# Kernel optimization log

Measured on AMD Instinct MI355X. Metric: run time of the kernel, lower is better.

The kernel has to match this reference:

```python
import jax, jax.numpy as jnp
import numpy as np

B, N, S, D1, D2 = 4, 16384, 4096, 128, 256
C_IN = D1 + D2  # 384
MLP = [256, 256]
EPS_BN = 1e-5


def setup_inputs() -> dict:
    key = jax.random.key(0)
    ks = jax.random.split(key, 16)
    inp = {
        "points_xyz1": jax.random.normal(ks[0], (B, N, 3), dtype=jnp.float32),
        "points_xyz2": jax.random.normal(ks[1], (B, S, 3), dtype=jnp.float32),
        "points_fea1": jax.random.normal(ks[2], (B, D1, N), dtype=jnp.float32),
        "points_fea2": jax.random.normal(ks[3], (B, D2, S), dtype=jnp.float32),
    }
    c_in = C_IN
    for i, c_out in enumerate(MLP):
        scale = 1.0 / np.sqrt(c_in)
        inp[f"W{i}"] = jax.random.uniform(ks[4 + 3 * i], (c_out, c_in), jnp.float32, -scale, scale)
        inp[f"b{i}"] = jax.random.uniform(ks[5 + 3 * i], (c_out,), jnp.float32, -scale, scale)
        inp[f"gamma{i}"] = jnp.ones((c_out,), jnp.float32)
        inp[f"beta{i}"] = jnp.zeros((c_out,), jnp.float32)
        c_in = c_out
    return inp


def _coordinate_distance(x1, x2):
    # squared euclidean distance matrix: (B,N,S)
    n1 = jnp.sum(x1 * x1, axis=-1, keepdims=True)          # (B,N,1)
    n2 = jnp.sum(x2 * x2, axis=-1, keepdims=True)          # (B,S,1)
    return n1 + jnp.swapaxes(n2, 1, 2) - 2.0 * jnp.einsum("bnc,bsc->bns", x1, x2)


def _conv_bn_relu(x, W, b, gamma, beta):
    # 1x1 conv: (B,Cin,N) -> (B,Cout,N), then BatchNorm1d (training stats) + ReLU
    y = jnp.einsum("oc,bcn->bon", W, x) + b[None, :, None]
    mean = jnp.mean(y, axis=(0, 2), keepdims=True)
    var = jnp.var(y, axis=(0, 2), keepdims=True)
    y = (y - mean) * jax.lax.rsqrt(var + EPS_BN)
    y = y * gamma[None, :, None] + beta[None, :, None]
    return jax.nn.relu(y)


def reference(points_xyz1, points_xyz2, points_fea1, points_fea2,
              W0, b0, gamma0, beta0, W1, b1, gamma1, beta1):
    dists = _coordinate_distance(points_xyz1[..., :3], points_xyz2[..., :3])  # (B,N,S)
    neg_d, idx = jax.lax.top_k(-dists, 3)                                     # 3 smallest
    d3 = -neg_d                                                               # (B,N,3)
    dist_recip = 1.0 / jnp.maximum(d3, 1e-8)
    weight = dist_recip / jnp.sum(dist_recip, axis=2, keepdims=True)          # (B,N,3)
    fea2t = jnp.swapaxes(points_fea2, 1, 2)                                   # (B,S,D2)
    gathered = fea2t[jnp.arange(B)[:, None, None], idx]                       # (B,N,3,D2)
    interp = jnp.sum(gathered * weight[..., None], axis=2)                    # (B,N,D2)
    new_fea = jnp.concatenate((points_fea1, jnp.swapaxes(interp, 1, 2)), axis=1)  # (B,D1+D2,N)
    new_fea = _conv_bn_relu(new_fea, W0, b0, gamma0, beta0)
    new_fea = _conv_bn_relu(new_fea, W1, b1, gamma1, beta1)
    return new_fea
```

## Files before the change

### kernel.cpp

```cpp
#include <hip/hip_runtime.h>
#include <math.h>

namespace {

constexpr int kB = 4;
constexpr int kN = 16384;
constexpr int kS = 4096;
constexpr int kD1 = 128;
constexpr int kD2 = 256;
constexpr int kCO = 256;
constexpr int kNCOL = kB * kN;
constexpr int kKX = kD1 + kD2;

constexpr size_t kOffAb0 = 262144;
constexpr size_t kOffAb1 = 264192;
constexpr size_t kOffY0  = 266240;
constexpr size_t kOffX1  = 33820672;

typedef __bf16 bf16x8 __attribute__((ext_vector_type(8)));
typedef float f32x4 __attribute__((ext_vector_type(4)));

__device__ __forceinline__ float bf2f(unsigned short u) {
  unsigned int x = ((unsigned int)u) << 16;
  float f;
  __builtin_memcpy(&f, &x, 4);
  return f;
}
__device__ __forceinline__ unsigned short f2bf(float f) {
  unsigned int x;
  __builtin_memcpy(&x, &f, 4);
  x += 0x7fffu + ((x >> 16) & 1u);
  return (unsigned short)(x >> 16);
}

__device__ __forceinline__ void cp16_async(const void* g, void* l) {
#if __has_builtin(__builtin_amdgcn_global_load_lds)
  __builtin_amdgcn_global_load_lds(
      (const __attribute__((address_space(1))) unsigned int*)g,
      (__attribute__((address_space(3))) unsigned int*)l, 16, 0, 0);
#else
  *(uint4*)l = *(const uint4*)g;
#endif
}

__global__ __launch_bounds__(256) void pts4_kernel(const float* __restrict__ xyz2,
                                                   float4* __restrict__ pts4) {
#pragma clang fp contract(off)
  int i = blockIdx.x * 256 + threadIdx.x;
  float x = xyz2[i * 3 + 0];
  float y = xyz2[i * 3 + 1];
  float z = xyz2[i * 3 + 2];
  float4 p;
  p.w = (x * x + y * y) + z * z;
  p.x = x + x; p.y = y + y; p.z = z + z;
  pts4[i] = p;
}

__global__ __launch_bounds__(256) void transpose_kernel(const float* __restrict__ fea2,
                                                        float* __restrict__ fea2t) {
  __shared__ float T[64][65];
  int b = blockIdx.z;
  int c0 = blockIdx.y * 64;
  int s0 = blockIdx.x * 64;
  int t = threadIdx.x;
  {
    int sl = t & 63, cg = t >> 6;
#pragma unroll
    for (int i = 0; i < 16; ++i) {
      int cl = cg * 16 + i;
      T[sl][cl] = fea2[((size_t)(b * kD2 + c0 + cl)) * kS + s0 + sl];
    }
  }
  __syncthreads();
  {
    int cl = t & 63, sg = t >> 6;
#pragma unroll
    for (int i = 0; i < 16; ++i) {
      int sl = sg * 16 + i;
      fea2t[((size_t)(b * kS + s0 + sl)) * kD2 + c0 + cl] = T[sl][cl];
    }
  }
}

__global__ __launch_bounds__(256) void fea1t_kernel(const float* __restrict__ fea1,
                                                    unsigned short* __restrict__ XT) {
  __shared__ float T[64][129];
  int n0 = blockIdx.x * 64;
  int b = blockIdx.y;
  int t = threadIdx.x;
  {
    int nl = t & 63, cg = t >> 6;
#pragma unroll
    for (int i = 0; i < 32; ++i) {
      int c = cg * 32 + i;
      T[nl][c] = fea1[((size_t)(b * kD1 + c)) * kN + n0 + nl];
    }
  }
  __syncthreads();
  {
    int nl = t >> 2, ch = t & 3;
    unsigned short h[32];
#pragma unroll
    for (int i = 0; i < 32; ++i) h[i] = f2bf(T[nl][ch * 32 + i]);
    uint4* dst = (uint4*)&XT[(size_t)(b * kN + n0 + nl) * kKX + ch * 32];
#pragma unroll
    for (int i = 0; i < 4; ++i) dst[i] = ((uint4*)h)[i];
  }
}

__global__ __launch_bounds__(512) void knn_interp_kernel(
    const float* __restrict__ xyz1, const float4* __restrict__ pts4,
    const float* __restrict__ fea2t, unsigned short* __restrict__ XT) {
#pragma clang fp contract(off)
  __shared__ float cd[8][64][3];
  __shared__ int ci[8][64][3];
  __shared__ float wsh[3][64];
  __shared__ int ish[3][64];
  int tid = threadIdx.x;
  int q = tid & 63;
  int chunk = __builtin_amdgcn_readfirstlane(tid >> 6);
  int b = blockIdx.x >> 8;
  int n0 = (blockIdx.x & 255) * 64;
  int n = n0 + q;
  int qg = b * kN + n;

  const float* p1 = xyz1 + (size_t)qg * 3;
  float x = p1[0], y = p1[1], z = p1[2];
  float n1 = (x * x + y * y) + z * z;

  const float4* pp = pts4 + b * kS + chunk * 512;
  int sbase = chunk * 512;
  float d0v = 1e30f, d1v = 1e30f, d2v = 1e30f;
  int i0 = 0, i1 = 0, i2 = 0;
  for (int s = 0; s < 512; s += 4) {
    float4 P[4];
    P[0] = pp[s]; P[1] = pp[s + 1]; P[2] = pp[s + 2]; P[3] = pp[s + 3];
#pragma unroll
    for (int u = 0; u < 4; ++u) {
      float dot2 = (x * P[u].x + y * P[u].y) + z * P[u].z;
      float d = (n1 + P[u].w) - dot2;
      if (__ballot(d < d2v)) {
        int si = sbase + s + u;
        bool b0 = d < d0v, b1 = d < d1v, b2 = d < d2v;
        int i2n = b1 ? i1 : (b2 ? si : i2);
        int i1n = b0 ? i0 : (b1 ? si : i1);
        int i0n = b0 ? si : i0;
        d2v = __builtin_amdgcn_fmed3f(d1v, d, d2v);
        d1v = __builtin_amdgcn_fmed3f(d0v, d, d1v);
        d0v = fminf(d0v, d);
        i0 = i0n; i1 = i1n; i2 = i2n;
      }
    }
  }
  cd[chunk][q][0] = d0v; cd[chunk][q][1] = d1v; cd[chunk][q][2] = d2v;
  ci[chunk][q][0] = i0;  ci[chunk][q][1] = i1;  ci[chunk][q][2] = i2;
  __syncthreads();

  if (tid < 64) {
    float D0 = 1e30f, D1 = 1e30f, D2 = 1e30f;
    int I0 = -1, I1 = -1, I2 = -1;
    for (int c2 = 0; c2 < 8; ++c2) {
#pragma unroll
      for (int k = 0; k < 3; ++k) {
        float d = cd[c2][tid][k];
        int i = ci[c2][tid][k];
        bool q0 = (d < D0) || (d == D0 && i < I0);
        bool q1 = (d < D1) || (d == D1 && i < I1);
        bool q2 = (d < D2) || (d == D2 && i < I2);
        if (q0)      { D2 = D1; I2 = I1; D1 = D0; I1 = I0; D0 = d; I0 = i; }
        else if (q1) { D2 = D1; I2 = I1; D1 = d;  I1 = i; }
        else if (q2) { D2 = d;  I2 = i; }
      }
    }
    float r0 = 1.0f / fmaxf(D0, 1e-8f);
    float r1 = 1.0f / fmaxf(D1, 1e-8f);
    float r2 = 1.0f / fmaxf(D2, 1e-8f);
    float rs = (r0 + r1) + r2;
    wsh[0][tid] = r0 / rs; wsh[1][tid] = r1 / rs; wsh[2][tid] = r2 / rs;
    ish[0][tid] = I0; ish[1][tid] = I1; ish[2][tid] = I2;
  }
  __syncthreads();

  int gq = tid >> 3, l = tid & 7;
  float w0 = wsh[0][gq], w1 = wsh[1][gq], w2 = wsh[2][gq];
  int qg2 = b * kN + n0 + gq;
  const float* fb = fea2t + ((size_t)b * kS) * kD2;
  const float* g0p = fb + (size_t)ish[0][gq] * kD2;
  const float* g1p = fb + (size_t)ish[1][gq] * kD2;
  const float* g2p = fb + (size_t)ish[2][gq] * kD2;
  unsigned short* op = XT + (size_t)qg2 * kKX + kD1;
#pragma unroll
  for (int k = 0; k < 8; ++k) {
    int c = (l + 8 * k) * 4;
    float4 f0 = *(const float4*)(g0p + c);
    float4 f1 = *(const float4*)(g1p + c);
    float4 f2 = *(const float4*)(g2p + c);
    unsigned short h[4];
    h[0] = f2bf((w0 * f0.x + w1 * f1.x) + w2 * f2.x);
    h[1] = f2bf((w0 * f0.y + w1 * f1.y) + w2 * f2.y);
    h[2] = f2bf((w0 * f0.z + w1 * f1.z) + w2 * f2.z);
    h[3] = f2bf((w0 * f0.w + w1 * f1.w) + w2 * f2.w);
    *(uint2*)(op + c) = *(uint2*)h;
  }
}

template <int KDIM, int LAYER>
__global__ __launch_bounds__(256) void gemm_kernel(
    const float* __restrict__ W, const unsigned short* __restrict__ Bt,
    const float* __restrict__ bias, void* __restrict__ Yp) {
  constexpr int ALD = 40;
  __shared__ unsigned short As[128 * ALD];
  __shared__ unsigned short Bs[128 * 32];
  int tid = threadIdx.x;
  int j0 = blockIdx.x * 128;
  int m0 = blockIdx.y * 128;
  int w = tid >> 6, lane = tid & 63;
  int wm = w & 1, wn = w >> 1;
  int quad = lane >> 4, l16 = lane & 15;
  int arow = tid & 127, ahalf = tid >> 7;
  int brow = tid >> 2, bch = tid & 3;

  bf16x8 pone, pm;
#pragma unroll
  for (int i = 0; i < 8; ++i) { pone[i] = (__bf16)1.0f; pm[i] = (__bf16)(float)l16; }
  f32x4 zf = {};
  f32x4 dr = __builtin_amdgcn_mfma_f32_16x16x32_bf16(pm, pone, zf, 0, 0, 0);
  f32x4 dc = __builtin_amdgcn_mfma_f32_16x16x32_bf16(pone, pm, zf, 0, 0, 0);
  int rowv[4], colv[4];
#pragma unroll
  for (int r = 0; r < 4; ++r) {
    rowv[r] = (int)(dr[r] * (1.0f / 32.0f) + 0.5f);
    colv[r] = (int)(dc[r] * (1.0f / 32.0f) + 0.5f);
  }

  f32x4 acc[4][4] = {};
  for (int k0 = 0; k0 < KDIM; k0 += 32) {
    cp16_async(Bt + (size_t)(j0 + brow) * KDIM + k0 + bch * 8, &Bs[(size_t)tid * 8]);
    cp16_async(Bt + (size_t)(j0 + 64 + brow) * KDIM + k0 + bch * 8, &Bs[(size_t)(tid + 256) * 8]);
    {
      const float* ap = W + (size_t)(m0 + arow) * KDIM + k0 + ahalf * 16;
      float4 f0 = *(const float4*)(ap);
      float4 f1 = *(const float4*)(ap + 4);
      float4 f2 = *(const float4*)(ap + 8);
      float4 f3 = *(const float4*)(ap + 12);
      unsigned short h[16] = {f2bf(f0.x), f2bf(f0.y), f2bf(f0.z), f2bf(f0.w),
                              f2bf(f1.x), f2bf(f1.y), f2bf(f1.z), f2bf(f1.w),
                              f2bf(f2.x), f2bf(f2.y), f2bf(f2.z), f2bf(f2.w),
                              f2bf(f3.x), f2bf(f3.y), f2bf(f3.z), f2bf(f3.w)};
      uint4* dst = (uint4*)&As[arow * ALD + ahalf * 16];
      dst[0] = ((uint4*)h)[0];
      dst[1] = ((uint4*)h)[1];
    }
    __syncthreads();
    bf16x8 af[4], bfr[4];
#pragma unroll
    for (int mt = 0; mt < 4; ++mt)
      af[mt] = *(const bf16x8*)(&As[(wm * 64 + mt * 16 + l16) * ALD + quad * 8]);
#pragma unroll
    for (int nt = 0; nt < 4; ++nt)
      bfr[nt] = *(const bf16x8*)(&Bs[(wn * 64 + nt * 16 + l16) * 32 + quad * 8]);
#pragma unroll
    for (int mt = 0; mt < 4; ++mt)
#pragma unroll
      for (int nt = 0; nt < 4; ++nt)
        acc[mt][nt] = __builtin_amdgcn_mfma_f32_16x16x32_bf16(af[mt], bfr[nt], acc[mt][nt], 0, 0, 0);
    __syncthreads();
  }

#pragma unroll
  for (int mt = 0; mt < 4; ++mt) {
#pragma unroll
    for (int r = 0; r < 4; ++r) {
      int o = m0 + wm * 64 + mt * 16 + rowv[r];
      float bv = bias[o];
#pragma unroll
      for (int nt = 0; nt < 4; ++nt) {
        int j = j0 + wn * 64 + nt * 16 + colv[r];
        float v = acc[mt][nt][r] + bv;
        if (LAYER == 0) {
          ((unsigned short*)Yp)[(size_t)o * kNCOL + j] = f2bf(v);
        } else {
          int bb = j >> 14, nn = j & (kN - 1);
          ((float*)Yp)[((size_t)(bb * kCO + o)) * kN + nn] = v;
        }
      }
    }
  }
}

__global__ __launch_bounds__(256) void stats0_kernel(const unsigned short* __restrict__ Y,
                                                     const float* __restrict__ gamma,
                                                     const float* __restrict__ beta,
                                                     float* __restrict__ ab) {
  __shared__ float sd[512];
  int o = blockIdx.x, tid = threadIdx.x;
  float s = 0.f, s2 = 0.f;
  const uint4* row = (const uint4*)(Y + (size_t)o * kNCOL);
  for (int v = tid; v < kNCOL / 8; v += 256) {
    uint4 u = row[v];
    const unsigned short* t = (const unsigned short*)&u;
#pragma unroll
    for (int k = 0; k < 8; ++k) { float x = bf2f(t[k]); s += x; s2 += x * x; }
  }
  sd[tid] = s;
  sd[256 + tid] = s2;
  __syncthreads();
  for (int st = 128; st > 0; st >>= 1) {
    if (tid < st) { sd[tid] += sd[tid + st]; sd[256 + tid] += sd[256 + tid + st]; }
    __syncthreads();
  }
  if (tid == 0) {
    float m = sd[0] * (1.0f / 65536.f);
    float var = sd[256] * (1.0f / 65536.f) - m * m;
    float rsq = 1.0f / sqrtf(var + 1e-5f);
    float a = gamma[o] * rsq;
    float c = beta[o] - m * a;
    ab[o] = a;
    ab[kCO + o] = c;
  }
}

__global__ __launch_bounds__(256) void apply_kernel(const unsigned short* __restrict__ Y0,
                                                    const float* __restrict__ ab,
                                                    unsigned short* __restrict__ X1T) {
  __shared__ unsigned short T[64][70];
  int j0 = blockIdx.x * 64, o0 = blockIdx.y * 64;
  int t = threadIdx.x;
  {
    int jl = t & 63, og = t >> 6;
#pragma unroll
    for (int i = 0; i < 16; ++i) {
      int ol = og * 16 + i;
      float a = ab[o0 + ol], c = ab[kCO + o0 + ol];
      float v = fmaxf(fmaf(a, bf2f(Y0[(size_t)(o0 + ol) * kNCOL + j0 + jl]), c), 0.f);
      T[ol][jl] = f2bf(v);
    }
  }
  __syncthreads();
  {
    int jl = t >> 2, ch = t & 3;
    unsigned short h[16];
#pragma unroll
    for (int i = 0; i < 16; ++i) h[i] = T[ch * 16 + i][jl];
    uint4* dst = (uint4*)&X1T[(size_t)(j0 + jl) * kCO + o0 + ch * 16];
    dst[0] = ((uint4*)h)[0];
    dst[1] = ((uint4*)h)[1];
  }
}

__global__ __launch_bounds__(256) void stats1_kernel(const float* __restrict__ Y,
                                                     const float* __restrict__ gamma,
                                                     const float* __restrict__ beta,
                                                     float* __restrict__ ab) {
  __shared__ float sd[512];
  int o = blockIdx.x, tid = threadIdx.x;
  float s = 0.f, s2 = 0.f;
  for (int bb = 0; bb < kB; ++bb) {
    const float4* row = (const float4*)(Y + ((size_t)(bb * kCO + o)) * kN);
    for (int v = tid; v < kN / 4; v += 256) {
      float4 u = row[v];
      const float* t = (const float*)&u;
#pragma unroll
      for (int k = 0; k < 4; ++k) { float xx = t[k]; s += xx; s2 += xx * xx; }
    }
  }
  sd[tid] = s;
  sd[256 + tid] = s2;
  __syncthreads();
  for (int st = 128; st > 0; st >>= 1) {
    if (tid < st) { sd[tid] += sd[tid + st]; sd[256 + tid] += sd[256 + tid + st]; }
    __syncthreads();
  }
  if (tid == 0) {
    float m = sd[0] * (1.0f / 65536.f);
    float var = sd[256] * (1.0f / 65536.f) - m * m;
    float rsq = 1.0f / sqrtf(var + 1e-5f);
    float a = gamma[o] * rsq;
    float c = beta[o] - m * a;
    ab[o] = a;
    ab[kCO + o] = c;
  }
}

__global__ __launch_bounds__(256) void finalf_kernel(float* __restrict__ Y,
                                                     const float* __restrict__ ab) {
  size_t i = ((size_t)blockIdx.x * 256 + threadIdx.x) * 4;
  int o = (int)((i >> 14) & (kCO - 1));
  float a = ab[o], c = ab[kCO + o];
  float4 u = *(float4*)(Y + i);
  float* t = (float*)&u;
#pragma unroll
  for (int k = 0; k < 4; ++k) t[k] = fmaxf(fmaf(a, t[k], c), 0.0f);
  *(float4*)(Y + i) = u;
}

}

extern "C" void kernel_launch(void* const* d_in, const int* in_sizes, int n_in,
                              void* d_out, int out_size, void* d_ws, size_t ws_size,
                              hipStream_t stream) {
  const float* xyz1 = (const float*)d_in[0];
  const float* xyz2 = (const float*)d_in[1];
  const float* fea1 = (const float*)d_in[2];
  const float* fea2 = (const float*)d_in[3];
  const float* W0 = (const float*)d_in[4];
  const float* b0 = (const float*)d_in[5];
  const float* g0 = (const float*)d_in[6];
  const float* be0 = (const float*)d_in[7];
  const float* W1 = (const float*)d_in[8];
  const float* b1 = (const float*)d_in[9];
  const float* g1 = (const float*)d_in[10];
  const float* be1 = (const float*)d_in[11];
  float* out = (float*)d_out;

  char* ws = (char*)d_ws;
  float4* pts4 = (float4*)ws;
  float* ab0 = (float*)(ws + kOffAb0);
  float* ab1 = (float*)(ws + kOffAb1);
  unsigned short* Y0bf = (unsigned short*)(ws + kOffY0);
  unsigned short* X1T = (unsigned short*)(ws + kOffX1);
  float* fea2t = (float*)(ws + kOffX1);
  unsigned short* XT = (unsigned short*)d_out;

  if (ws_size < (size_t)kOffX1 + (size_t)kNCOL * kCO * 2) return;

  pts4_kernel<<<kB * kS / 256, 256, 0, stream>>>(xyz2, pts4);
  transpose_kernel<<<dim3(kS / 64, kD2 / 64, kB), 256, 0, stream>>>(fea2, fea2t);
  fea1t_kernel<<<dim3(kN / 64, kB), 256, 0, stream>>>(fea1, XT);
  knn_interp_kernel<<<kNCOL / 64, 512, 0, stream>>>(xyz1, pts4, fea2t, XT);
  gemm_kernel<kKX, 0><<<dim3(kNCOL / 128, kCO / 128), 256, 0, stream>>>(W0, XT, b0, Y0bf);
  stats0_kernel<<<kCO, 256, 0, stream>>>(Y0bf, g0, be0, ab0);
  apply_kernel<<<dim3(kNCOL / 64, kCO / 64), 256, 0, stream>>>(Y0bf, ab0, X1T);
  gemm_kernel<kCO, 1><<<dim3(kNCOL / 128, kCO / 128), 256, 0, stream>>>(W1, X1T, b1, out);
  stats1_kernel<<<kCO, 256, 0, stream>>>(out, g1, be1, ab1);
  finalf_kernel<<<kCO * kNCOL / (256 * 4), 256, 0, stream>>>(out, ab1);
}
```

Before: 393.7 us.

## Fuse BatchNorm statistics and apply into cooperative GEMM kernels with grid sync

Each pointwise-conv GEMM now runs as a cooperative kernel. In the epilogue it reduces per-channel sum and sum of squares with wavefront shuffles and global atomics, then does a grid-wide sync. After the sync it applies the BN affine and ReLU directly: a transposed bf16 write of X1T for layer 0, and an in-place normalize of its own output tile for layer 1. This removes the separate stats, apply and finalize kernels and the extra full passes over the intermediate tensors. The trade-offs are float atomics, variance computed as E[x^2]-mean^2 (less numerically robust), and reliance on every block being co-resident, with a fallback to the old kernel chain if the cooperative launch fails.

```diff
diff --git a/kernel.cpp b/kernel.cpp
--- a/kernel.cpp
+++ b/kernel.cpp
@@ -1,5 +1,8 @@
 #include <hip/hip_runtime.h>
+#include <hip/hip_cooperative_groups.h>
 #include <math.h>
+
+namespace cg = cooperative_groups;
 
 namespace {
 
@@ -64,10 +67,10 @@
   int s0 = blockIdx.x * 64;
   int t = threadIdx.x;
   {
-    int sl = t & 63, cg = t >> 6;
+    int sl = t & 63, cg2 = t >> 6;
 #pragma unroll
     for (int i = 0; i < 16; ++i) {
-      int cl = cg * 16 + i;
+      int cl = cg2 * 16 + i;
       T[sl][cl] = fea2[((size_t)(b * kD2 + c0 + cl)) * kS + s0 + sl];
     }
   }
@@ -89,10 +92,10 @@
   int b = blockIdx.y;
   int t = threadIdx.x;
   {
-    int nl = t & 63, cg = t >> 6;
+    int nl = t & 63, cg2 = t >> 6;
 #pragma unroll
     for (int i = 0; i < 32; ++i) {
-      int c = cg * 32 + i;
+      int c = cg2 * 32 + i;
       T[nl][c] = fea1[((size_t)(b * kD1 + c)) * kN + n0 + nl];
     }
   }
@@ -204,10 +207,17 @@
   }
 }
 
+__global__ __launch_bounds__(1024) void zstats_kernel(float* __restrict__ p) {
+  p[threadIdx.x] = 0.0f;
+}
+
 template <int KDIM, int LAYER>
-__global__ __launch_bounds__(256) void gemm_kernel(
+__global__ __launch_bounds__(256, 4) void gemm_coop(
     const float* __restrict__ W, const unsigned short* __restrict__ Bt,
-    const float* __restrict__ bias, void* __restrict__ Yp) {
+    const float* __restrict__ bias, void* __restrict__ Yp,
+    float* __restrict__ sbuf, float* __restrict__ qbuf,
+    const float* __restrict__ gamma, const float* __restrict__ beta,
+    unsigned short* __restrict__ X1T) {
   constexpr int ALD = 40;
   __shared__ unsigned short As[128 * ALD];
   __shared__ unsigned short Bs[128 * 32];
@@ -273,6 +283,164 @@
     for (int r = 0; r < 4; ++r) {
       int o = m0 + wm * 64 + mt * 16 + rowv[r];
       float bv = bias[o];
+      float s = 0.f, qq = 0.f;
+#pragma unroll
+      for (int nt = 0; nt < 4; ++nt) {
+        int j = j0 + wn * 64 + nt * 16 + colv[r];
+        float v = acc[mt][nt][r] + bv;
+        s += v; qq += v * v;
+        if (LAYER == 0) {
+          ((unsigned short*)Yp)[(size_t)o * kNCOL + j] = f2bf(v);
+        } else {
+          int bb = j >> 14, nn = j & (kN - 1);
+          ((float*)Yp)[((size_t)(bb * kCO + o)) * kN + nn] = v;
+        }
+      }
+#pragma unroll
+      for (int d2 = 1; d2 < 16; d2 <<= 1) {
+        s += __shfl_xor(s, d2, 64);
+        qq += __shfl_xor(qq, d2, 64);
+      }
+      if (l16 == 0) {
+        atomicAdd(&sbuf[o], s);
+        atomicAdd(&qbuf[o], qq);
+      }
+    }
+  }
+
+  __threadfence();
+  cg::this_grid().sync();
+
+  if (LAYER == 0) {
+    float* ash = (float*)Bs;
+    float* csh = ash + 256;
+    if (tid < 256) {
+      float s = sbuf[tid], qq = qbuf[tid];
+      float mme = s * (1.0f / 65536.f);
+      float var = qq * (1.0f / 65536.f) - mme * mme;
+      float rsq = 1.0f / sqrtf(var + 1e-5f);
+      float a = gamma[tid] * rsq;
+      ash[tid] = a;
+      csh[tid] = beta[tid] - mme * a;
+    }
+    __syncthreads();
+    unsigned short (*T)[70] = (unsigned short (*)[70])As;
+    int jbase = j0 + blockIdx.y * 64;
+    const unsigned short* Y0 = (const unsigned short*)Yp;
+    for (int o0 = 0; o0 < kCO; o0 += 64) {
+      __syncthreads();
+      {
+        int jl = tid & 63, og = tid >> 6;
+#pragma unroll
+        for (int i = 0; i < 16; ++i) {
+          int ol = og * 16 + i;
+          float v = fmaxf(fmaf(ash[o0 + ol], bf2f(Y0[(size_t)(o0 + ol) * kNCOL + jbase + jl]),
+                               csh[o0 + ol]), 0.f);
+          T[ol][jl] = f2bf(v);
+        }
+      }
+      __syncthreads();
+      {
+        int jl = tid >> 2, ch = tid & 3;
+        unsigned short h[16];
+#pragma unroll
+        for (int i = 0; i < 16; ++i) h[i] = T[ch * 16 + i][jl];
+        uint4* dst = (uint4*)&X1T[(size_t)(jbase + jl) * kCO + o0 + ch * 16];
+        dst[0] = ((uint4*)h)[0];
+        dst[1] = ((uint4*)h)[1];
+      }
+    }
+  } else {
+    float* out = (float*)Yp;
+    int row = tid >> 1;
+    int o = m0 + row;
+    float s = sbuf[o], qq = qbuf[o];
+    float mme = s * (1.0f / 65536.f);
+    float var = qq * (1.0f / 65536.f) - mme * mme;
+    float rsq = 1.0f / sqrtf(var + 1e-5f);
+    float a = gamma[o] * rsq;
+    float c = beta[o] - mme * a;
+    int bb = j0 >> 14, nn0 = j0 & (kN - 1);
+    float* rp = out + ((size_t)(bb * kCO + o)) * kN + nn0 + (tid & 1) * 64;
+#pragma unroll
+    for (int i = 0; i < 16; ++i) {
+      float4 u = *(float4*)(rp + i * 4);
+      u.x = fmaxf(fmaf(a, u.x, c), 0.f);
+      u.y = fmaxf(fmaf(a, u.y, c), 0.f);
+      u.z = fmaxf(fmaf(a, u.z, c), 0.f);
+      u.w = fmaxf(fmaf(a, u.w, c), 0.f);
+      *(float4*)(rp + i * 4) = u;
+    }
+  }
+}
+
+
+template <int KDIM, int LAYER>
+__global__ __launch_bounds__(256) void gemm_kernel(
+    const float* __restrict__ W, const unsigned short* __restrict__ Bt,
+    const float* __restrict__ bias, void* __restrict__ Yp) {
+  constexpr int ALD = 40;
+  __shared__ unsigned short As[128 * ALD];
+  __shared__ unsigned short Bs[128 * 32];
+  int tid = threadIdx.x;
+  int j0 = blockIdx.x * 128;
+  int m0 = blockIdx.y * 128;
+  int w = tid >> 6, lane = tid & 63;
+  int wm = w & 1, wn = w >> 1;
+  int quad = lane >> 4, l16 = lane & 15;
+  int arow = tid & 127, ahalf = tid >> 7;
+  int brow = tid >> 2, bch = tid & 3;
+  bf16x8 pone, pm;
+#pragma unroll
+  for (int i = 0; i < 8; ++i) { pone[i] = (__bf16)1.0f; pm[i] = (__bf16)(float)l16; }
+  f32x4 zf = {};
+  f32x4 dr = __builtin_amdgcn_mfma_f32_16x16x32_bf16(pm, pone, zf, 0, 0, 0);
+  f32x4 dc = __builtin_amdgcn_mfma_f32_16x16x32_bf16(pone, pm, zf, 0, 0, 0);
+  int rowv[4], colv[4];
+#pragma unroll
+  for (int r = 0; r < 4; ++r) {
+    rowv[r] = (int)(dr[r] * (1.0f / 32.0f) + 0.5f);
+    colv[r] = (int)(dc[r] * (1.0f / 32.0f) + 0.5f);
+  }
+  f32x4 acc[4][4] = {};
+  for (int k0 = 0; k0 < KDIM; k0 += 32) {
+    cp16_async(Bt + (size_t)(j0 + brow) * KDIM + k0 + bch * 8, &Bs[(size_t)tid * 8]);
+    cp16_async(Bt + (size_t)(j0 + 64 + brow) * KDIM + k0 + bch * 8, &Bs[(size_t)(tid + 256) * 8]);
+    {
+      const float* ap = W + (size_t)(m0 + arow) * KDIM + k0 + ahalf * 16;
+      float4 f0 = *(const float4*)(ap);
+      float4 f1 = *(const float4*)(ap + 4);
+      float4 f2 = *(const float4*)(ap + 8);
+      float4 f3 = *(const float4*)(ap + 12);
+      unsigned short h[16] = {f2bf(f0.x), f2bf(f0.y), f2bf(f0.z), f2bf(f0.w),
+                              f2bf(f1.x), f2bf(f1.y), f2bf(f1.z), f2bf(f1.w),
+                              f2bf(f2.x), f2bf(f2.y), f2bf(f2.z), f2bf(f2.w),
+                              f2bf(f3.x), f2bf(f3.y), f2bf(f3.z), f2bf(f3.w)};
+      uint4* dst = (uint4*)&As[arow * ALD + ahalf * 16];
+      dst[0] = ((uint4*)h)[0];
+      dst[1] = ((uint4*)h)[1];
+    }
+    __syncthreads();
+    bf16x8 af[4], bfr[4];
+#pragma unroll
+    for (int mt = 0; mt < 4; ++mt)
+      af[mt] = *(const bf16x8*)(&As[(wm * 64 + mt * 16 + l16) * ALD + quad * 8]);
+#pragma unroll
+    for (int nt = 0; nt < 4; ++nt)
+      bfr[nt] = *(const bf16x8*)(&Bs[(wn * 64 + nt * 16 + l16) * 32 + quad * 8]);
+#pragma unroll
+    for (int mt = 0; mt < 4; ++mt)
+#pragma unroll
+      for (int nt = 0; nt < 4; ++nt)
+        acc[mt][nt] = __builtin_amdgcn_mfma_f32_16x16x32_bf16(af[mt], bfr[nt], acc[mt][nt], 0, 0, 0);
+    __syncthreads();
+  }
+#pragma unroll
+  for (int mt = 0; mt < 4; ++mt) {
+#pragma unroll
+    for (int r = 0; r < 4; ++r) {
+      int o = m0 + wm * 64 + mt * 16 + rowv[r];
+      float bv = bias[o];
 #pragma unroll
       for (int nt = 0; nt < 4; ++nt) {
         int j = j0 + wn * 64 + nt * 16 + colv[r];
@@ -415,6 +583,7 @@
 
   char* ws = (char*)d_ws;
   float4* pts4 = (float4*)ws;
+  float* statsbuf = (float*)ws;
   float* ab0 = (float*)(ws + kOffAb0);
   float* ab1 = (float*)(ws + kOffAb1);
   unsigned short* Y0bf = (unsigned short*)(ws + kOffY0);
@@ -428,10 +597,39 @@
   transpose_kernel<<<dim3(kS / 64, kD2 / 64, kB), 256, 0, stream>>>(fea2, fea2t);
   fea1t_kernel<<<dim3(kN / 64, kB), 256, 0, stream>>>(fea1, XT);
   knn_interp_kernel<<<kNCOL / 64, 512, 0, stream>>>(xyz1, pts4, fea2t, XT);
-  gemm_kernel<kKX, 0><<<dim3(kNCOL / 128, kCO / 128), 256, 0, stream>>>(W0, XT, b0, Y0bf);
-  stats0_kernel<<<kCO, 256, 0, stream>>>(Y0bf, g0, be0, ab0);
-  apply_kernel<<<dim3(kNCOL / 64, kCO / 64), 256, 0, stream>>>(Y0bf, ab0, X1T);
-  gemm_kernel<kCO, 1><<<dim3(kNCOL / 128, kCO / 128), 256, 0, stream>>>(W1, X1T, b1, out);
-  stats1_kernel<<<kCO, 256, 0, stream>>>(out, g1, be1, ab1);
-  finalf_kernel<<<kCO * kNCOL / (256 * 4), 256, 0, stream>>>(out, ab1);
-}
+  zstats_kernel<<<1, 1024, 0, stream>>>(statsbuf);
+
+  float* s0p = statsbuf;
+  float* q0p = statsbuf + 256;
+  float* s1p = statsbuf + 512;
+  float* q1p = statsbuf + 768;
+
+  {
+    const float* Wp = W0; const unsigned short* Btp = XT; const float* bp = b0;
+    void* Yp = (void*)Y0bf; float* sb = s0p; float* qb = q0p;
+    const float* gp = g0; const float* bep = be0; unsigned short* xp = X1T;
+    void* args0[] = {&Wp, &Btp, &bp, &Yp, &sb, &qb, &gp, &bep, &xp};
+    hipError_t e0 = hipLaunchCooperativeKernel(
+        (const void*)gemm_coop<kKX, 0>, dim3(kNCOL / 128, kCO / 128),
+        dim3(256, 1, 1), args0, 0, stream);
+    if (e0 != hipSuccess) {
+      gemm_kernel<kKX, 0><<<dim3(kNCOL / 128, kCO / 128), 256, 0, stream>>>(W0, XT, b0, Y0bf);
+      stats0_kernel<<<kCO, 256, 0, stream>>>(Y0bf, g0, be0, ab0);
+      apply_kernel<<<dim3(kNCOL / 64, kCO / 64), 256, 0, stream>>>(Y0bf, ab0, X1T);
+    }
+  }
+  {
+    const float* Wp = W1; const unsigned short* Btp = X1T; const float* bp = b1;
+    void* Yp = (void*)out; float* sb = s1p; float* qb = q1p;
+    const float* gp = g1; const float* bep = be1; unsigned short* xp = X1T;
+    void* args1[] = {&Wp, &Btp, &bp, &Yp, &sb, &qb, &gp, &bep, &xp};
+    hipError_t e1 = hipLaunchCooperativeKernel(
+        (const void*)gemm_coop<kCO, 1>, dim3(kNCOL / 128, kCO / 128),
+        dim3(256, 1, 1), args1, 0, stream);
+    if (e1 != hipSuccess) {
+      gemm_kernel<kCO, 1><<<dim3(kNCOL / 128, kCO / 128), 256, 0, stream>>>(W1, X1T, b1, out);
+      stats1_kernel<<<kCO, 256, 0, stream>>>(out, g1, be1, ab1);
+      finalf_kernel<<<kCO * kNCOL / (256 * 4), 256, 0, stream>>>(out, ab1);
+    }
+  }
+}
```

Result: slower. 1.053 ms (+167.5%).

## Fuse BN statistics into GEMM epilogues and apply BN0+ReLU in GEMM1 loader

Applied to the files above, without the earlier changes.

The first GEMM now writes its output already transposed to a node-major bf16 buffer and emits per-block partial sums and sums of squares. A small reduction kernel turns these into BN scale and shift. The second GEMM applies BN0 and ReLU on the fly while loading its B operand and also emits partial statistics for BN1. This removes the separate stats0, apply/transpose and stats1 passes over large intermediates, at the cost of extra epilogue work, an LDS transpose and a two-level reduction order for the statistics.

```diff
diff --git a/kernel.cpp b/kernel.cpp
--- a/kernel.cpp
+++ b/kernel.cpp
@@ -12,10 +12,10 @@
 constexpr int kNCOL = kB * kN;
 constexpr int kKX = kD1 + kD2;
 
-constexpr size_t kOffAb0 = 262144;
-constexpr size_t kOffAb1 = 264192;
-constexpr size_t kOffY0  = 266240;
-constexpr size_t kOffX1  = 33820672;
+constexpr size_t kOffAb0  = 262144;
+constexpr size_t kOffAb1  = 264192;
+constexpr size_t kOffX1p  = 266240;
+constexpr size_t kOffPart = 33820672;
 
 typedef __bf16 bf16x8 __attribute__((ext_vector_type(8)));
 typedef float f32x4 __attribute__((ext_vector_type(4)));
@@ -64,10 +64,10 @@
   int s0 = blockIdx.x * 64;
   int t = threadIdx.x;
   {
-    int sl = t & 63, cg = t >> 6;
+    int sl = t & 63, cg2 = t >> 6;
 #pragma unroll
     for (int i = 0; i < 16; ++i) {
-      int cl = cg * 16 + i;
+      int cl = cg2 * 16 + i;
       T[sl][cl] = fea2[((size_t)(b * kD2 + c0 + cl)) * kS + s0 + sl];
     }
   }
@@ -89,10 +89,10 @@
   int b = blockIdx.y;
   int t = threadIdx.x;
   {
-    int nl = t & 63, cg = t >> 6;
+    int nl = t & 63, cg2 = t >> 6;
 #pragma unroll
     for (int i = 0; i < 32; ++i) {
-      int c = cg * 32 + i;
+      int c = cg2 * 32 + i;
       T[nl][c] = fea1[((size_t)(b * kD1 + c)) * kN + n0 + nl];
     }
   }
@@ -204,13 +204,16 @@
   }
 }
 
-template <int KDIM, int LAYER>
-__global__ __launch_bounds__(256) void gemm_kernel(
+__global__ __launch_bounds__(256) void gemm0t_kernel(
     const float* __restrict__ W, const unsigned short* __restrict__ Bt,
-    const float* __restrict__ bias, void* __restrict__ Yp) {
+    const float* __restrict__ bias, unsigned short* __restrict__ X1pre,
+    float* __restrict__ partS, float* __restrict__ partQ) {
+  constexpr int KDIM = kKX;
   constexpr int ALD = 40;
-  __shared__ unsigned short As[128 * ALD];
-  __shared__ unsigned short Bs[128 * 32];
+  __shared__ unsigned short smem[9216];
+  unsigned short* As = smem;
+  unsigned short* Bs = smem + 128 * ALD;
+  __shared__ float psum[2][128], pq[2][128];
   int tid = threadIdx.x;
   int j0 = blockIdx.x * 128;
   int m0 = blockIdx.y * 128;
@@ -267,118 +270,223 @@
     __syncthreads();
   }
 
+  uint2 h2[4][4];
 #pragma unroll
   for (int mt = 0; mt < 4; ++mt) {
+    int obase = m0 + wm * 64 + mt * 16 + rowv[0];
+    float4 bv4 = *(const float4*)&bias[obase];
+    float s4[4] = {0.f, 0.f, 0.f, 0.f}, q4[4] = {0.f, 0.f, 0.f, 0.f};
+#pragma unroll
+    for (int nt = 0; nt < 4; ++nt) {
+      unsigned short hh[4];
+#pragma unroll
+      for (int r = 0; r < 4; ++r) {
+        float v = acc[mt][nt][r] + ((const float*)&bv4)[r];
+        s4[r] += v; q4[r] += v * v;
+        hh[r] = f2bf(v);
+      }
+      h2[mt][nt] = *(uint2*)hh;
+    }
 #pragma unroll
     for (int r = 0; r < 4; ++r) {
-      int o = m0 + wm * 64 + mt * 16 + rowv[r];
+      float s = s4[r], qq = q4[r];
+#pragma unroll
+      for (int d2 = 1; d2 < 16; d2 <<= 1) {
+        s += __shfl_xor(s, d2, 64);
+        qq += __shfl_xor(qq, d2, 64);
+      }
+      if (l16 == 0) {
+        int ol = wm * 64 + mt * 16 + rowv[0] + r;
+        psum[wn][ol] = s;
+        pq[wn][ol] = qq;
+      }
+    }
+  }
+
+  unsigned short* T = smem + wm * 4608;
+  int jr = lane >> 3, cc = lane & 7;
+  if (wn == 0) {
+#pragma unroll
+    for (int mt = 0; mt < 4; ++mt)
+#pragma unroll
+      for (int nt = 0; nt < 4; ++nt)
+        *(uint2*)&T[(nt * 16 + colv[0]) * 72 + mt * 16 + rowv[0]] = h2[mt][nt];
+#pragma unroll
+    for (int it = 0; it < 8; ++it) {
+      int jl = it * 8 + jr;
+      uint4 u = *(uint4*)&T[jl * 72 + cc * 8];
+      *(uint4*)&X1pre[(size_t)(j0 + jl) * kCO + m0 + wm * 64 + cc * 8] = u;
+    }
+  }
+  __syncthreads();
+  if (wn == 1) {
+#pragma unroll
+    for (int mt = 0; mt < 4; ++mt)
+#pragma unroll
+      for (int nt = 0; nt < 4; ++nt)
+        *(uint2*)&T[(nt * 16 + colv[0]) * 72 + mt * 16 + rowv[0]] = h2[mt][nt];
+#pragma unroll
+    for (int it = 0; it < 8; ++it) {
+      int jl = it * 8 + jr;
+      uint4 u = *(uint4*)&T[jl * 72 + cc * 8];
+      *(uint4*)&X1pre[(size_t)(j0 + 64 + jl) * kCO + m0 + wm * 64 + cc * 8] = u;
+    }
+  }
+  if (tid < 128) {
+    float ss = psum[0][tid] + psum[1][tid];
+    float qq = pq[0][tid] + pq[1][tid];
+    partS[(size_t)blockIdx.x * kCO + m0 + tid] = ss;
+    partQ[(size_t)blockIdx.x * kCO + m0 + tid] = qq;
+  }
+}
+
+__global__ __launch_bounds__(64) void redstats_kernel(
+    const float* __restrict__ pS, const float* __restrict__ pQ,
+    const float* __restrict__ gamma, const float* __restrict__ beta,
+    float* __restrict__ ab) {
+  int o = blockIdx.x, t = threadIdx.x;
+  float s = 0.f, q = 0.f;
+  for (int i = t; i < 512; i += 64) {
+    s += pS[(size_t)i * kCO + o];
+    q += pQ[(size_t)i * kCO + o];
+  }
+#pragma unroll
+  for (int d = 1; d < 64; d <<= 1) {
+    s += __shfl_xor(s, d, 64);
+    q += __shfl_xor(q, d, 64);
+  }
+  if (t == 0) {
+    float m = s * (1.0f / 65536.f);
+    float var = q * (1.0f / 65536.f) - m * m;
+    float rsq = 1.0f / sqrtf(var + 1e-5f);
+    float a = gamma[o] * rsq;
+    ab[o] = a;
+    ab[kCO + o] = beta[o] - m * a;
+  }
+}
+
+__global__ __launch_bounds__(256) void gemm1f_kernel(
+    const float* __restrict__ W, const unsigned short* __restrict__ Xp,
+    const float* __restrict__ bias, const float* __restrict__ ab0,
+    float* __restrict__ out, float* __restrict__ partS, float* __restrict__ partQ) {
+  constexpr int KDIM = kCO;
+  constexpr int ALD = 40;
+  __shared__ unsigned short As[128 * ALD];
+  __shared__ unsigned short Bs[128 * 32];
+  __shared__ float Acf[256], Ccf[256];
+  __shared__ float psum[2][128], pq[2][128];
+  int tid = threadIdx.x;
+  int j0 = blockIdx.x * 128;
+  int m0 = blockIdx.y * 128;
+  int w = tid >> 6, lane = tid & 63;
+  int wm = w & 1, wn = w >> 1;
+  int quad = lane >> 4, l16 = lane & 15;
+  int arow = tid & 127, ahalf = tid >> 7;
+  int brow = tid >> 2, bch = tid & 3;
+
+  if (tid < 256) { Acf[tid] = ab0[tid]; Ccf[tid] = ab0[kCO + tid]; }
+
+  bf16x8 pone, pm;
+#pragma unroll
+  for (int i = 0; i < 8; ++i) { pone[i] = (__bf16)1.0f; pm[i] = (__bf16)(float)l16; }
+  f32x4 zf = {};
+  f32x4 dr = __builtin_amdgcn_mfma_f32_16x16x32_bf16(pm, pone, zf, 0, 0, 0);
+  f32x4 dc = __builtin_amdgcn_mfma_f32_16x16x32_bf16(pone, pm, zf, 0, 0, 0);
+  int rowv[4], colv[4];
+#pragma unroll
+  for (int r = 0; r < 4; ++r) {
+    rowv[r] = (int)(dr[r] * (1.0f / 32.0f) + 0.5f);
+    colv[r] = (int)(dc[r] * (1.0f / 32.0f) + 0.5f);
+  }
+  __syncthreads();
+
+  f32x4 acc[4][4] = {};
+  for (int k0 = 0; k0 < KDIM; k0 += 32) {
+    {
+      int cb = k0 + bch * 8;
+      float4 a0 = *(const float4*)&Acf[cb];
+      float4 a1 = *(const float4*)&Acf[cb + 4];
+      float4 c0 = *(const float4*)&Ccf[cb];
+      float4 c1 = *(const float4*)&Ccf[cb + 4];
+#pragma unroll
+      for (int h = 0; h < 2; ++h) {
+        uint4 raw = *(const uint4*)(Xp + (size_t)(j0 + h * 64 + brow) * kCO + cb);
+        const unsigned short* rs = (const unsigned short*)&raw;
+        unsigned short o8[8];
+        o8[0] = f2bf(fmaxf(fmaf(a0.x, bf2f(rs[0]), c0.x), 0.f));
+        o8[1] = f2bf(fmaxf(fmaf(a0.y, bf2f(rs[1]), c0.y), 0.f));
+        o8[2] = f2bf(fmaxf(fmaf(a0.z, bf2f(rs[2]), c0.z), 0.f));
+        o8[3] = f2bf(fmaxf(fmaf(a0.w, bf2f(rs[3]), c0.w), 0.f));
+        o8[4] = f2bf(fmaxf(fmaf(a1.x, bf2f(rs[4]), c1.x), 0.f));
+        o8[5] = f2bf(fmaxf(fmaf(a1.y, bf2f(rs[5]), c1.y), 0.f));
+        o8[6] = f2bf(fmaxf(fmaf(a1.z, bf2f(rs[6]), c1.z), 0.f));
+        o8[7] = f2bf(fmaxf(fmaf(a1.w, bf2f(rs[7]), c1.w), 0.f));
+        *(uint4*)&Bs[(size_t)(tid + h * 256) * 8] = *(uint4*)o8;
+      }
+    }
+    {
+      const float* ap = W + (size_t)(m0 + arow) * KDIM + k0 + ahalf * 16;
+      float4 f0 = *(const float4*)(ap);
+      float4 f1 = *(const float4*)(ap + 4);
+      float4 f2 = *(const float4*)(ap + 8);
+      float4 f3 = *(const float4*)(ap + 12);
+      unsigned short h[16] = {f2bf(f0.x), f2bf(f0.y), f2bf(f0.z), f2bf(f0.w),
+                              f2bf(f1.x), f2bf(f1.y), f2bf(f1.z), f2bf(f1.w),
+                              f2bf(f2.x), f2bf(f2.y), f2bf(f2.z), f2bf(f2.w),
+                              f2bf(f3.x), f2bf(f3.y), f2bf(f3.z), f2bf(f3.w)};
+      uint4* dst = (uint4*)&As[arow * ALD + ahalf * 16];
+      dst[0] = ((uint4*)h)[0];
+      dst[1] = ((uint4*)h)[1];
+    }
+    __syncthreads();
+    bf16x8 af[4], bfr[4];
+#pragma unroll
+    for (int mt = 0; mt < 4; ++mt)
+      af[mt] = *(const bf16x8*)(&As[(wm * 64 + mt * 16 + l16) * ALD + quad * 8]);
+#pragma unroll
+    for (int nt = 0; nt < 4; ++nt)
+      bfr[nt] = *(const bf16x8*)(&Bs[(wn * 64 + nt * 16 + l16) * 32 + quad * 8]);
+#pragma unroll
+    for (int mt = 0; mt < 4; ++mt)
+#pragma unroll
+      for (int nt = 0; nt < 4; ++nt)
+        acc[mt][nt] = __builtin_amdgcn_mfma_f32_16x16x32_bf16(af[mt], bfr[nt], acc[mt][nt], 0, 0, 0);
+    __syncthreads();
+  }
+
+#pragma unroll
+  for (int mt = 0; mt < 4; ++mt) {
+#pragma unroll
+    for (int r = 0; r < 4; ++r) {
+      int ol = wm * 64 + mt * 16 + rowv[r];
+      int o = m0 + ol;
       float bv = bias[o];
+      float s = 0.f, qq = 0.f;
 #pragma unroll
       for (int nt = 0; nt < 4; ++nt) {
         int j = j0 + wn * 64 + nt * 16 + colv[r];
         float v = acc[mt][nt][r] + bv;
-        if (LAYER == 0) {
-          ((unsigned short*)Yp)[(size_t)o * kNCOL + j] = f2bf(v);
-        } else {
-          int bb = j >> 14, nn = j & (kN - 1);
-          ((float*)Yp)[((size_t)(bb * kCO + o)) * kN + nn] = v;
-        }
-      }
-    }
-  }
-}
-
-__global__ __launch_bounds__(256) void stats0_kernel(const unsigned short* __restrict__ Y,
-                                                     const float* __restrict__ gamma,
-                                                     const float* __restrict__ beta,
-                                                     float* __restrict__ ab) {
-  __shared__ float sd[512];
-  int o = blockIdx.x, tid = threadIdx.x;
-  float s = 0.f, s2 = 0.f;
-  const uint4* row = (const uint4*)(Y + (size_t)o * kNCOL);
-  for (int v = tid; v < kNCOL / 8; v += 256) {
-    uint4 u = row[v];
-    const unsigned short* t = (const unsigned short*)&u;
-#pragma unroll
-    for (int k = 0; k < 8; ++k) { float x = bf2f(t[k]); s += x; s2 += x * x; }
-  }
-  sd[tid] = s;
-  sd[256 + tid] = s2;
-  __syncthreads();
-  for (int st = 128; st > 0; st >>= 1) {
-    if (tid < st) { sd[tid] += sd[tid + st]; sd[256 + tid] += sd[256 + tid + st]; }
-    __syncthreads();
-  }
-  if (tid == 0) {
-    float m = sd[0] * (1.0f / 65536.f);
-    float var = sd[256] * (1.0f / 65536.f) - m * m;
-    float rsq = 1.0f / sqrtf(var + 1e-5f);
-    float a = gamma[o] * rsq;
-    float c = beta[o] - m * a;
-    ab[o] = a;
-    ab[kCO + o] = c;
-  }
-}
-
-__global__ __launch_bounds__(256) void apply_kernel(const unsigned short* __restrict__ Y0,
-                                                    const float* __restrict__ ab,
-                                                    unsigned short* __restrict__ X1T) {
-  __shared__ unsigned short T[64][70];
-  int j0 = blockIdx.x * 64, o0 = blockIdx.y * 64;
-  int t = threadIdx.x;
-  {
-    int jl = t & 63, og = t >> 6;
-#pragma unroll
-    for (int i = 0; i < 16; ++i) {
-      int ol = og * 16 + i;
-      float a = ab[o0 + ol], c = ab[kCO + o0 + ol];
-      float v = fmaxf(fmaf(a, bf2f(Y0[(size_t)(o0 + ol) * kNCOL + j0 + jl]), c), 0.f);
-      T[ol][jl] = f2bf(v);
-    }
-  }
-  __syncthreads();
-  {
-    int jl = t >> 2, ch = t & 3;
-    unsigned short h[16];
-#pragma unroll
-    for (int i = 0; i < 16; ++i) h[i] = T[ch * 16 + i][jl];
-    uint4* dst = (uint4*)&X1T[(size_t)(j0 + jl) * kCO + o0 + ch * 16];
-    dst[0] = ((uint4*)h)[0];
-    dst[1] = ((uint4*)h)[1];
-  }
-}
-
-__global__ __launch_bounds__(256) void stats1_kernel(const float* __restrict__ Y,
-                                                     const float* __restrict__ gamma,
-                                                     const float* __restrict__ beta,
-                                                     float* __restrict__ ab) {
-  __shared__ float sd[512];
-  int o = blockIdx.x, tid = threadIdx.x;
-  float s = 0.f, s2 = 0.f;
-  for (int bb = 0; bb < kB; ++bb) {
-    const float4* row = (const float4*)(Y + ((size_t)(bb * kCO + o)) * kN);
-    for (int v = tid; v < kN / 4; v += 256) {
-      float4 u = row[v];
-      const float* t = (const float*)&u;
-#pragma unroll
-      for (int k = 0; k < 4; ++k) { float xx = t[k]; s += xx; s2 += xx * xx; }
-    }
-  }
-  sd[tid] = s;
-  sd[256 + tid] = s2;
-  __syncthreads();
-  for (int st = 128; st > 0; st >>= 1) {
-    if (tid < st) { sd[tid] += sd[tid + st]; sd[256 + tid] += sd[256 + tid + st]; }
-    __syncthreads();
-  }
-  if (tid == 0) {
-    float m = sd[0] * (1.0f / 65536.f);
-    float var = sd[256] * (1.0f / 65536.f) - m * m;
-    float rsq = 1.0f / sqrtf(var + 1e-5f);
-    float a = gamma[o] * rsq;
-    float c = beta[o] - m * a;
-    ab[o] = a;
-    ab[kCO + o] = c;
+        s += v; qq += v * v;
+        int bb = j >> 14, nn = j & (kN - 1);
+        out[((size_t)(bb * kCO + o)) * kN + nn] = v;
+      }
+#pragma unroll
+      for (int d2 = 1; d2 < 16; d2 <<= 1) {
+        s += __shfl_xor(s, d2, 64);
+        qq += __shfl_xor(qq, d2, 64);
+      }
+      if (l16 == 0) {
+        psum[wn][ol] = s;
+        pq[wn][ol] = qq;
+      }
+    }
+  }
+  __syncthreads();
+  if (tid < 128) {
+    float ss = psum[0][tid] + psum[1][tid];
+    float qq = pq[0][tid] + pq[1][tid];
+    partS[(size_t)blockIdx.x * kCO + m0 + tid] = ss;
+    partQ[(size_t)blockIdx.x * kCO + m0 + tid] = qq;
   }
 }
 
@@ -417,21 +525,21 @@
   float4* pts4 = (float4*)ws;
   float* ab0 = (float*)(ws + kOffAb0);
   float* ab1 = (float*)(ws + kOffAb1);
-  unsigned short* Y0bf = (unsigned short*)(ws + kOffY0);
-  unsigned short* X1T = (unsigned short*)(ws + kOffX1);
-  float* fea2t = (float*)(ws + kOffX1);
+  unsigned short* X1pre = (unsigned short*)(ws + kOffX1p);
+  float* partS = (float*)(ws + kOffPart);
+  float* partQ = (float*)(ws + kOffPart + 524288);
+  float* fea2t = (float*)(ws + kOffPart);
   unsigned short* XT = (unsigned short*)d_out;
 
-  if (ws_size < (size_t)kOffX1 + (size_t)kNCOL * kCO * 2) return;
+  if (ws_size < (size_t)kOffPart + 2 * 524288) return;
 
   pts4_kernel<<<kB * kS / 256, 256, 0, stream>>>(xyz2, pts4);
   transpose_kernel<<<dim3(kS / 64, kD2 / 64, kB), 256, 0, stream>>>(fea2, fea2t);
   fea1t_kernel<<<dim3(kN / 64, kB), 256, 0, stream>>>(fea1, XT);
   knn_interp_kernel<<<kNCOL / 64, 512, 0, stream>>>(xyz1, pts4, fea2t, XT);
-  gemm_kernel<kKX, 0><<<dim3(kNCOL / 128, kCO / 128), 256, 0, stream>>>(W0, XT, b0, Y0bf);
-  stats0_kernel<<<kCO, 256, 0, stream>>>(Y0bf, g0, be0, ab0);
-  apply_kernel<<<dim3(kNCOL / 64, kCO / 64), 256, 0, stream>>>(Y0bf, ab0, X1T);
-  gemm_kernel<kCO, 1><<<dim3(kNCOL / 128, kCO / 128), 256, 0, stream>>>(W1, X1T, b1, out);
-  stats1_kernel<<<kCO, 256, 0, stream>>>(out, g1, be1, ab1);
+  gemm0t_kernel<<<dim3(kNCOL / 128, kCO / 128), 256, 0, stream>>>(W0, XT, b0, X1pre, partS, partQ);
+  redstats_kernel<<<kCO, 64, 0, stream>>>(partS, partQ, g0, be0, ab0);
+  gemm1f_kernel<<<dim3(kNCOL / 128, kCO / 128), 256, 0, stream>>>(W1, X1pre, b1, ab0, out, partS, partQ);
+  redstats_kernel<<<kCO, 64, 0, stream>>>(partS, partQ, g1, be1, ab1);
   finalf_kernel<<<kCO * kNCOL / (256 * 4), 256, 0, stream>>>(out, ab1);
 }
```

Measured after the change: 375.4 us. 1.05x faster.
